# Kernel optimization log

Measured on AMD Instinct MI355X. Metric: run time of the kernel, lower is better.

## Reference

```python
import jax, jax.numpy as jnp
import numpy as np

DIM = 1024
HEADS = 16
HEAD_DIM = DIM // HEADS
B, N = 4, 4096


def setup_inputs() -> dict:
    key = jax.random.key(0)
    ks = jax.random.split(key, 10)
    s = 1.0 / np.sqrt(DIM)
    return {
        "x": jax.random.normal(ks[0], (B, N, DIM), dtype=jnp.float32),
        "Wq": jax.random.uniform(ks[1], (DIM, DIM), jnp.float32, -s, s),
        "bq": jax.random.uniform(ks[2], (DIM,), jnp.float32, -s, s),
        "Wk": jax.random.uniform(ks[3], (DIM, DIM), jnp.float32, -s, s),
        "bk": jax.random.uniform(ks[4], (DIM,), jnp.float32, -s, s),
        "Wv": jax.random.uniform(ks[5], (DIM, DIM), jnp.float32, -s, s),
        "bv": jax.random.uniform(ks[6], (DIM,), jnp.float32, -s, s),
        "Wo": jax.random.uniform(ks[7], (DIM, DIM), jnp.float32, -s, s),
        "bo": jax.random.uniform(ks[8], (DIM,), jnp.float32, -s, s),
        "stdp": jnp.ones((HEADS,), dtype=jnp.float32),
    }


def reference(x, Wq, bq, Wk, bk, Wv, bv, Wo, bo, stdp):
    b, n, d = x.shape
    h, dh = HEADS, HEAD_DIM
    # projections (torch Linear: x @ W.T + b)
    def proj(W, bias):
        return (x @ W.T + bias).reshape(b, n, h, dh).transpose(0, 2, 1, 3)  # bhnd
    Q = jax.nn.elu(proj(Wq, bq)) + 1.0
    K = jax.nn.elu(proj(Wk, bk)) + 1.0
    V = proj(Wv, bv)
    stdp_w = jax.nn.sigmoid(stdp).reshape(1, h, 1, 1)
    KV = jnp.einsum('bhnd,bhnv->bhdv', K, V)      # (b,h,dh,dh)
    K_sum = K.sum(axis=2)                          # (b,h,dh)
    numerator = jnp.einsum('bhnd,bhdv->bhnv', Q, KV)
    denominator = jnp.einsum('bhnd,bhd->bhn', Q, K_sum)[..., None] + 1e-6
    attn_out = numerator / denominator * stdp_w    # (b,h,n,dh)
    out = attn_out.transpose(0, 2, 1, 3).reshape(b, n, d)
    out = out @ Wo.T + bo
    return (out, jax.lax.stop_gradient(stdp))
```

## Files before the change

### kernel.cpp

```cpp
#include <hip/hip_runtime.h>
#include <hip/hip_bf16.h>

#define DIMSZ 1024
#define SEQLEN 4096
#define NHEAD 16
#define NX 16777216L
#define NW 1048576L
#define KVSPLITS 8

typedef __attribute__((ext_vector_type(8))) short bf16x8;
typedef __attribute__((ext_vector_type(4))) float f32x4;

__device__ __forceinline__ unsigned short f2bf(float f) {
    union { float f; unsigned int i; } c; c.f = f;
    unsigned int x = c.i;
    unsigned int r = (x + 0x7fffu + ((x >> 16) & 1u)) >> 16;
    return (unsigned short)r;
}

__device__ __forceinline__ unsigned int pk2(float lo, float hi) {
    union { float f; unsigned int i; } a, b; a.f = lo; b.f = hi;
    return __builtin_amdgcn_perm(b.i + 0x8000u, a.i + 0x8000u, 0x07060302u);
}

__device__ __forceinline__ void unp8r(bf16x8 v, float* f) {
    union { bf16x8 s; uint4 w; } u; u.s = v;
    union { unsigned int i; float f; } c;
    c.i = u.w.x << 16;           f[0] = c.f;
    c.i = u.w.x & 0xffff0000u;   f[1] = c.f;
    c.i = u.w.y << 16;           f[2] = c.f;
    c.i = u.w.y & 0xffff0000u;   f[3] = c.f;
    c.i = u.w.z << 16;           f[4] = c.f;
    c.i = u.w.z & 0xffff0000u;   f[5] = c.f;
    c.i = u.w.w << 16;           f[6] = c.f;
    c.i = u.w.w & 0xffff0000u;   f[7] = c.f;
}

__device__ __forceinline__ void async16(const void* g, void* l) {
    __builtin_amdgcn_global_load_lds(
        (const __attribute__((address_space(1))) void*)g,
        (__attribute__((address_space(3))) void*)l,
        16, 0, 0);
}

__global__ __launch_bounds__(256) void cast_pack(
    const float* __restrict__ x, const float* __restrict__ Wq,
    const float* __restrict__ Wk, const float* __restrict__ Wv,
    const float* __restrict__ Wo, const float* __restrict__ stdp,
    unsigned short* __restrict__ xb, unsigned short* __restrict__ Wqkv,
    unsigned short* __restrict__ Wob, float* __restrict__ outTail)
{
    long i4 = ((long)blockIdx.x * 256 + threadIdx.x) * 4;
    const float* src; unsigned short* dst; long off;
    if (i4 < NX)               { src = x;  dst = xb;          off = i4; }
    else if (i4 < NX + NW)     { src = Wq; dst = Wqkv;        off = i4 - NX; }
    else if (i4 < NX + 2*NW)   { src = Wk; dst = Wqkv + NW;   off = i4 - NX - NW; }
    else if (i4 < NX + 3*NW)   { src = Wv; dst = Wqkv + 2*NW; off = i4 - NX - 2*NW; }
    else                       { src = Wo; dst = Wob;         off = i4 - NX - 3*NW; }
    float4 v = *(const float4*)(src + off);
    union { unsigned short u[4]; uint2 p; } o;
    o.u[0] = f2bf(v.x); o.u[1] = f2bf(v.y); o.u[2] = f2bf(v.z); o.u[3] = f2bf(v.w);
    *(uint2*)(dst + off) = o.p;
    if (blockIdx.x == 0 && threadIdx.x < NHEAD) outTail[threadIdx.x] = stdp[threadIdx.x];
}

__global__ __launch_bounds__(1024, 1) void qkv_gemm8(
    const unsigned short* __restrict__ A, const unsigned short* __restrict__ W,
    const float* __restrict__ bq, const float* __restrict__ bk,
    const float* __restrict__ bv,
    unsigned short* __restrict__ Qb, unsigned short* __restrict__ Kb,
    unsigned short* __restrict__ Vb)
{
    __shared__ __align__(16) char SM[131072];
    const int t = threadIdx.x;
    const int wave = t >> 6, lane = t & 63;
    const int lr = lane & 15, lq = lane >> 4;
    const int wm = wave >> 2, wn = wave & 3;
    const int m0 = blockIdx.x * 256;
    const int c0 = blockIdx.y * 256;

    const int sc = (((t & 7) ^ ((t >> 3) & 7)) * 8);
    const unsigned short* pA = A + (long)(m0 + (t >> 3)) * DIMSZ + sc;
    const unsigned short* pB = W + (long)(c0 + (t >> 3)) * DIMSZ + sc;
    char* ldsW = SM + wave * 1024;

    const int xo = ((lq ^ (lr & 7)) << 4);
    const char* ABase = SM + wm * 8192 + lr * 128;
    const char* BBase = SM + 32768 + (wn * 64 + lr) * 128;

    f32x4 acc[4][4];
    #pragma unroll
    for (int i = 0; i < 4; ++i)
        #pragma unroll
        for (int j = 0; j < 4; ++j) acc[i][j] = (f32x4){0.f, 0.f, 0.f, 0.f};

#define STAGE(Q, O) do {                                                        \
        if ((Q) < 16) {                                                         \
            const int isB_ = ((O) < 2) ? 1 : 0;                                 \
            const int half_ = isB_ ? (O) : ((O) - 2);                           \
            const unsigned short* s_ = (isB_ ? pB : pA)                         \
                                       + (long)half_ * 131072 + (Q) * 64;       \
            char* d_ = ldsW + (((Q) & 1) << 16) + isB_ * 32768 + half_ * 16384; \
            async16(s_, d_);                                                    \
        }                                                                       \
    } while (0)

    STAGE(0, 0); STAGE(0, 1); STAGE(0, 2); STAGE(0, 3);
    STAGE(1, 0); STAGE(1, 1); STAGE(1, 2);
    asm volatile("s_waitcnt vmcnt(3)" ::: "memory");
    __builtin_amdgcn_s_barrier();

    for (int kt = 0; kt < 16; ++kt) {
        const int buf = (kt & 1) << 16;
        bf16x8 a[4], b[4];

        b[0] = *(const bf16x8*)(BBase + buf + 0 * 2048 + xo);
        b[1] = *(const bf16x8*)(BBase + buf + 1 * 2048 + xo);
        #pragma unroll
        for (int i = 0; i < 4; ++i)
            a[i] = *(const bf16x8*)(ABase + buf + i * 2048 + xo);
        __builtin_amdgcn_sched_barrier(0);
        b[2] = *(const bf16x8*)(BBase + buf + 2 * 2048 + xo);
        b[3] = *(const bf16x8*)(BBase + buf + 3 * 2048 + xo);
        __builtin_amdgcn_sched_barrier(0);
        STAGE(kt + 1, 3);

        asm volatile("s_waitcnt lgkmcnt(2)" ::: "memory");
        __builtin_amdgcn_sched_barrier(0);
        __builtin_amdgcn_s_setprio(1);
        #pragma unroll
        for (int i = 0; i < 4; ++i)
            #pragma unroll
            for (int j = 0; j < 2; ++j)
                acc[i][j] = __builtin_amdgcn_mfma_f32_16x16x32_bf16(
                    b[j], a[i], acc[i][j], 0, 0, 0);
        __builtin_amdgcn_s_setprio(0);

        asm volatile("s_waitcnt lgkmcnt(0)" ::: "memory");
        __builtin_amdgcn_sched_barrier(0);
        __builtin_amdgcn_s_setprio(1);
        #pragma unroll
        for (int i = 0; i < 4; ++i)
            #pragma unroll
            for (int j = 2; j < 4; ++j)
                acc[i][j] = __builtin_amdgcn_mfma_f32_16x16x32_bf16(
                    b[j], a[i], acc[i][j], 0, 0, 0);
        __builtin_amdgcn_s_setprio(0);

        b[0] = *(const bf16x8*)(BBase + buf + 0 * 2048 + (xo ^ 64));
        b[1] = *(const bf16x8*)(BBase + buf + 1 * 2048 + (xo ^ 64));
        #pragma unroll
        for (int i = 0; i < 4; ++i)
            a[i] = *(const bf16x8*)(ABase + buf + i * 2048 + (xo ^ 64));
        __builtin_amdgcn_sched_barrier(0);
        b[2] = *(const bf16x8*)(BBase + buf + 2 * 2048 + (xo ^ 64));
        b[3] = *(const bf16x8*)(BBase + buf + 3 * 2048 + (xo ^ 64));
        __builtin_amdgcn_sched_barrier(0);

        asm volatile("s_waitcnt lgkmcnt(2)" ::: "memory");
        __builtin_amdgcn_sched_barrier(0);
        __builtin_amdgcn_s_setprio(1);
        #pragma unroll
        for (int i = 0; i < 4; ++i)
            #pragma unroll
            for (int j = 0; j < 2; ++j)
                acc[i][j] = __builtin_amdgcn_mfma_f32_16x16x32_bf16(
                    b[j], a[i], acc[i][j], 0, 0, 0);
        __builtin_amdgcn_s_setprio(0);

        asm volatile("s_waitcnt lgkmcnt(0)" ::: "memory");
        __builtin_amdgcn_sched_barrier(0);
        __builtin_amdgcn_s_barrier();
        STAGE(kt + 2, 0); STAGE(kt + 2, 1); STAGE(kt + 2, 2);

        __builtin_amdgcn_s_setprio(1);
        #pragma unroll
        for (int i = 0; i < 4; ++i)
            #pragma unroll
            for (int j = 2; j < 4; ++j)
                acc[i][j] = __builtin_amdgcn_mfma_f32_16x16x32_bf16(
                    b[j], a[i], acc[i][j], 0, 0, 0);
        __builtin_amdgcn_s_setprio(0);

        if (kt < 14)       asm volatile("s_waitcnt vmcnt(3)" ::: "memory");
        else if (kt == 14) asm volatile("s_waitcnt vmcnt(0)" ::: "memory");
        __builtin_amdgcn_s_barrier();
    }
#undef STAGE

    const int proj = c0 >> 10;
    const float* bias = proj == 0 ? bq : (proj == 1 ? bk : bv);
    const bool qk = proj < 2;
    const int cb = (c0 & 1023) + wn * 64;
    const int q4 = lq * 4;
    #pragma unroll
    for (int j = 0; j < 4; ++j) {
        const float4 b4 = *(const float4*)(bias + cb + 16 * j + q4);
        #pragma unroll
        for (int i = 0; i < 4; ++i) {
            float v0 = acc[i][j][0] + b4.x, v1 = acc[i][j][1] + b4.y;
            float v2 = acc[i][j][2] + b4.z, v3 = acc[i][j][3] + b4.w;
            if (qk) {
                v0 = v0 > 0.f ? v0 + 1.f : __expf(v0);
                v1 = v1 > 0.f ? v1 + 1.f : __expf(v1);
                v2 = v2 > 0.f ? v2 + 1.f : __expf(v2);
                v3 = v3 > 0.f ? v3 + 1.f : __expf(v3);
            }
            const int row = wm * 64 + 16 * i + lr;
            int byte = row * 512 + wn * 128 + j * 32 + q4 * 2;
            byte ^= (row & 7) << 4;
            uint2 pkd; pkd.x = pk2(v0, v1); pkd.y = pk2(v2, v3);
            *(uint2*)(SM + byte) = pkd;
        }
    }
    __syncthreads();
    unsigned short* dstp = proj == 0 ? Qb : (proj == 1 ? Kb : Vb);
    const int colsh = (t & 31) * 8;
    const int h = ((c0 >> 6) + (colsh >> 6)) & 15;
    const int b_ = m0 >> 12;
    unsigned short* dbase = dstp + ((long)(b_ * 16 + h) * SEQLEN) * 64 + (colsh & 63);
    #pragma unroll
    for (int u = 0; u < 8; ++u) {
        const int flat = u * 16384 + t * 16;
        const int row = flat >> 9;
        uint4 val = *(const uint4*)(SM + (flat ^ ((row & 7) << 4)));
        const int n = (m0 + row) & 4095;
        *(uint4*)(dbase + (long)n * 64) = val;
    }
}

__global__ __launch_bounds__(256) void kv_reduce(
    const unsigned short* __restrict__ Kb, const unsigned short* __restrict__ Vb,
    float* __restrict__ KVp, float* __restrict__ Ksump)
{
    __shared__ __align__(16) char LDS[65536];
    int bh = blockIdx.x, split = blockIdx.y, t = threadIdx.x;
    int wave = t >> 6, lane = t & 63, lr = lane & 15, lq = lane >> 4;

    const int nl = t & 127;
    const int dh = (t >> 7) * 32;
    const int vrow = 16 * wave + lr;

    f32x4 acc[4];
    #pragma unroll
    for (int j = 0; j < 4; ++j) acc[j] = (f32x4){0.f, 0.f, 0.f, 0.f};
    float ksp[4] = {0.f, 0.f, 0.f, 0.f};

    for (int half = 0; half < 2; ++half) {
        const unsigned short* Kbase = Kb + ((long)bh * SEQLEN + split * 512 + half * 256) * 64;
        const unsigned short* Vbase = Vb + ((long)bh * SEQLEN + split * 512 + half * 256) * 64;

        union Q2S { uint4 q[4]; unsigned short s[32]; };
        Q2S kq[2], vq[2];
        #pragma unroll
        for (int it = 0; it < 2; ++it) {
            const unsigned short* kp = Kbase + (long)(it * 128 + nl) * 64 + dh;
            const unsigned short* vp = Vbase + (long)(it * 128 + nl) * 64 + dh;
            #pragma unroll
            for (int g = 0; g < 4; ++g) {
                kq[it].q[g] = *(const uint4*)(kp + g * 8);
                vq[it].q[g] = *(const uint4*)(vp + g * 8);
            }
        }
        if (half) __syncthreads();
        #pragma unroll
        for (int it = 0; it < 2; ++it) {
            char* buf = LDS + it * 32768;
            #pragma unroll
            for (int e = 0; e < 32; ++e) {
                const int d = dh + e;
                const int a = d * 256 + ((nl * 2) ^ ((d & 7) << 4));
                *(unsigned short*)(buf + a) = kq[it].s[e];
                *(unsigned short*)(buf + 16384 + a) = vq[it].s[e];
            }
        }
        __syncthreads();

        #pragma unroll
        for (int it = 0; it < 2; ++it) {
            const char* buf = LDS + it * 32768;
            #pragma unroll
            for (int ns = 0; ns < 4; ++ns) {
                const int xoff = (ns * 64 + lq * 16) ^ ((lr & 7) << 4);
                bf16x8 af = *(const bf16x8*)(buf + 16384 + vrow * 256 + xoff);
                bf16x8 bfr[4];
                #pragma unroll
                for (int j = 0; j < 4; ++j)
                    bfr[j] = *(const bf16x8*)(buf + (16 * j + lr) * 256 + xoff);
                if (wave == 0) {
                    #pragma unroll
                    for (int j = 0; j < 4; ++j) {
                        float kf[8]; unp8r(bfr[j], kf);
                        ksp[j] += ((kf[0] + kf[1]) + (kf[2] + kf[3]))
                                + ((kf[4] + kf[5]) + (kf[6] + kf[7]));
                    }
                }
                #pragma unroll
                for (int j = 0; j < 4; ++j)
                    acc[j] = __builtin_amdgcn_mfma_f32_16x16x32_bf16(bfr[j], af, acc[j], 0, 0, 0);
            }
        }
    }

    float* kp = KVp + ((long)split * 64 + bh) * 4096;
    const int q4 = lq * 4;
    #pragma unroll
    for (int j = 0; j < 4; ++j)
        *(f32x4*)(kp + vrow * 64 + 16 * j + q4) = acc[j];

    if (wave == 0) {
        #pragma unroll
        for (int j = 0; j < 4; ++j) {
            float s = ksp[j];
            s += __shfl_xor(s, 16);
            s += __shfl_xor(s, 32);
            if (lane < 16)
                Ksump[((long)split * 64 + bh) * 64 + 16 * j + lr] = s;
        }
    }
}

__global__ __launch_bounds__(256) void kv_final(
    const float* __restrict__ KVp, const float* __restrict__ Ksump,
    unsigned short* __restrict__ KVb, float* __restrict__ Ksum)
{
    int bh = blockIdx.x, t = threadIdx.x;
    float s[16];
    #pragma unroll
    for (int g = 0; g < 16; ++g) s[g] = 0.f;
    for (int sp = 0; sp < KVSPLITS; ++sp) {
        const float* src = KVp + ((long)sp * 64 + bh) * 4096 + t * 16;
        #pragma unroll
        for (int g = 0; g < 4; ++g) {
            float4 v = *(const float4*)(src + g * 4);
            s[g * 4 + 0] += v.x; s[g * 4 + 1] += v.y;
            s[g * 4 + 2] += v.z; s[g * 4 + 3] += v.w;
        }
    }
    uint4 o0, o1;
    o0.x = pk2(s[0], s[1]);  o0.y = pk2(s[2], s[3]);
    o0.z = pk2(s[4], s[5]);  o0.w = pk2(s[6], s[7]);
    o1.x = pk2(s[8], s[9]);  o1.y = pk2(s[10], s[11]);
    o1.z = pk2(s[12], s[13]); o1.w = pk2(s[14], s[15]);
    *(uint4*)(KVb + (long)bh * 4096 + t * 16) = o0;
    *(uint4*)(KVb + (long)bh * 4096 + t * 16 + 8) = o1;
    if (t < 16) {
        float4 a = {0.f, 0.f, 0.f, 0.f};
        for (int p = 0; p < KVSPLITS; p += 4) {
            #pragma unroll
            for (int q = 0; q < 4; ++q) {
                float4 v = *(const float4*)(Ksump + ((long)(p + q) * 64 + bh) * 64 + t * 4);
                a.x += v.x; a.y += v.y; a.z += v.z; a.w += v.w;
            }
        }
        *(float4*)(Ksum + bh * 64 + t * 4) = a;
    }
}

__global__ __launch_bounds__(256) void attn_kernel(
    const unsigned short* __restrict__ Qb, const unsigned short* __restrict__ KVb,
    const float* __restrict__ Ksum, const float* __restrict__ stdp,
    unsigned short* __restrict__ attn)
{
    __shared__ unsigned short Cs[256 * 72];
    int t = threadIdx.x;
    int bh = blockIdx.y;
    int b = bh >> 4, h = bh & 15;

    int wave = t >> 6, lane = t & 63, lr = lane & 15, lk = (lane >> 4) * 8;
    const unsigned short* kvb = KVb + (long)bh * 4096;
    const float* ksb = Ksum + bh * 64;

    bf16x8 bfrh[2][4];
    float ksf[2][8];
    #pragma unroll
    for (int s = 0; s < 2; ++s) {
        #pragma unroll
        for (int j = 0; j < 4; ++j)
            bfrh[s][j] = *(const bf16x8*)(kvb + (16 * j + lr) * 64 + s * 32 + lk);
        float4 ka = *(const float4*)(ksb + s * 32 + lk);
        float4 kb2 = *(const float4*)(ksb + s * 32 + lk + 4);
        ksf[s][0] = ka.x; ksf[s][1] = ka.y; ksf[s][2] = ka.z; ksf[s][3] = ka.w;
        ksf[s][4] = kb2.x; ksf[s][5] = kb2.y; ksf[s][6] = kb2.z; ksf[s][7] = kb2.w;
    }
    float sg = 1.f / (1.f + __expf(-stdp[h]));
    int q4 = (lane >> 4) * 4;

    for (int c = 0; c < 2; ++c) {
        int rc = blockIdx.x * 2 + c;
        int rowbase = rc * 256 + wave * 64;

        f32x4 acc[4][4];
        #pragma unroll
        for (int i = 0; i < 4; ++i)
            #pragma unroll
            for (int j = 0; j < 4; ++j) acc[i][j] = (f32x4){0.f, 0.f, 0.f, 0.f};
        float ds[4] = {0.f, 0.f, 0.f, 0.f};

        #pragma unroll
        for (int s = 0; s < 2; ++s) {
            bf16x8 af[4];
            #pragma unroll
            for (int i = 0; i < 4; ++i)
                af[i] = *(const bf16x8*)(Qb + ((long)bh * SEQLEN + rowbase + 16 * i + lr) * 64 + s * 32 + lk);
            #pragma unroll
            for (int i = 0; i < 4; ++i) {
                float qf[8]; unp8r(af[i], qf);
                #pragma unroll
                for (int e = 0; e < 8; ++e) ds[i] += qf[e] * ksf[s][e];
            }
            #pragma unroll
            for (int i = 0; i < 4; ++i)
                #pragma unroll
                for (int j = 0; j < 4; ++j)
                    acc[i][j] = __builtin_amdgcn_mfma_f32_16x16x32_bf16(bfrh[s][j], af[i], acc[i][j], 0, 0, 0);
        }

        float dinv_i[4];
        #pragma unroll
        for (int i = 0; i < 4; ++i) {
            float d = ds[i];
            d += __shfl_xor(d, 16);
            d += __shfl_xor(d, 32);
            dinv_i[i] = sg / (d + 1e-6f);
        }

        #pragma unroll
        for (int j = 0; j < 4; ++j) {
            int v0c = 16 * j + q4;
            #pragma unroll
            for (int i = 0; i < 4; ++i) {
                int row = wave * 64 + 16 * i + lr;
                float d = dinv_i[i];
                uint2 pkd;
                pkd.x = pk2(acc[i][j][0] * d, acc[i][j][1] * d);
                pkd.y = pk2(acc[i][j][2] * d, acc[i][j][3] * d);
                *(uint2*)(Cs + row * 72 + v0c) = pkd;
            }
        }
        __syncthreads();
        #pragma unroll
        for (int u = 0; u < 8; ++u) {
            int row = u * 32 + (t >> 3);
            int nn = rc * 256 + row;
            long a = ((long)(b * SEQLEN + nn)) * DIMSZ + h * 64 + (t & 7) * 8;
            *(uint4*)(attn + a) = *(const uint4*)(Cs + row * 72 + (t & 7) * 8);
        }
        __syncthreads();
    }
}

__global__ __launch_bounds__(1024, 1) void out_gemm8(
    const unsigned short* __restrict__ A, const unsigned short* __restrict__ W,
    const float* __restrict__ bo, float* __restrict__ out)
{
    __shared__ __align__(16) char SM[131072];
    const int t = threadIdx.x;
    const int wave = t >> 6, lane = t & 63;
    const int lr = lane & 15, lq = lane >> 4;
    const int wm = wave >> 2, wn = wave & 3;
    const int m0 = blockIdx.x * 256;
    const int c0 = blockIdx.y * 256;

    const int sc = (((t & 7) ^ ((t >> 3) & 7)) * 8);
    const unsigned short* pA = A + (long)(m0 + (t >> 3)) * DIMSZ + sc;
    const unsigned short* pB = W + (long)(c0 + (t >> 3)) * DIMSZ + sc;
    char* ldsW = SM + wave * 1024;

    const int xo = ((lq ^ (lr & 7)) << 4);
    const char* ABase = SM + wm * 8192 + lr * 128;
    const char* BBase = SM + 32768 + (wn * 64 + lr) * 128;

    f32x4 acc[4][4];
    #pragma unroll
    for (int i = 0; i < 4; ++i)
        #pragma unroll
        for (int j = 0; j < 4; ++j) acc[i][j] = (f32x4){0.f, 0.f, 0.f, 0.f};

#define STAGE(Q, O) do {                                                        \
        if ((Q) < 16) {                                                         \
            const int isB_ = ((O) < 2) ? 1 : 0;                                 \
            const int half_ = isB_ ? (O) : ((O) - 2);                           \
            const unsigned short* s_ = (isB_ ? pB : pA)                         \
                                       + (long)half_ * 131072 + (Q) * 64;       \
            char* d_ = ldsW + (((Q) & 1) << 16) + isB_ * 32768 + half_ * 16384; \
            async16(s_, d_);                                                    \
        }                                                                       \
    } while (0)

    STAGE(0, 0); STAGE(0, 1); STAGE(0, 2); STAGE(0, 3);
    STAGE(1, 0); STAGE(1, 1); STAGE(1, 2);
    asm volatile("s_waitcnt vmcnt(3)" ::: "memory");
    __builtin_amdgcn_s_barrier();

    for (int kt = 0; kt < 16; ++kt) {
        const int buf = (kt & 1) << 16;
        bf16x8 a[4], b[4];

        b[0] = *(const bf16x8*)(BBase + buf + 0 * 2048 + xo);
        b[1] = *(const bf16x8*)(BBase + buf + 1 * 2048 + xo);
        #pragma unroll
        for (int i = 0; i < 4; ++i)
            a[i] = *(const bf16x8*)(ABase + buf + i * 2048 + xo);
        __builtin_amdgcn_sched_barrier(0);
        b[2] = *(const bf16x8*)(BBase + buf + 2 * 2048 + xo);
        b[3] = *(const bf16x8*)(BBase + buf + 3 * 2048 + xo);
        __builtin_amdgcn_sched_barrier(0);
        STAGE(kt + 1, 3);

        asm volatile("s_waitcnt lgkmcnt(2)" ::: "memory");
        __builtin_amdgcn_sched_barrier(0);
        __builtin_amdgcn_s_setprio(1);
        #pragma unroll
        for (int i = 0; i < 4; ++i)
            #pragma unroll
            for (int j = 0; j < 2; ++j)
                acc[i][j] = __builtin_amdgcn_mfma_f32_16x16x32_bf16(
                    b[j], a[i], acc[i][j], 0, 0, 0);
        __builtin_amdgcn_s_setprio(0);

        asm volatile("s_waitcnt lgkmcnt(0)" ::: "memory");
        __builtin_amdgcn_sched_barrier(0);
        __builtin_amdgcn_s_setprio(1);
        #pragma unroll
        for (int i = 0; i < 4; ++i)
            #pragma unroll
            for (int j = 2; j < 4; ++j)
                acc[i][j] = __builtin_amdgcn_mfma_f32_16x16x32_bf16(
                    b[j], a[i], acc[i][j], 0, 0, 0);
        __builtin_amdgcn_s_setprio(0);

        b[0] = *(const bf16x8*)(BBase + buf + 0 * 2048 + (xo ^ 64));
        b[1] = *(const bf16x8*)(BBase + buf + 1 * 2048 + (xo ^ 64));
        #pragma unroll
        for (int i = 0; i < 4; ++i)
            a[i] = *(const bf16x8*)(ABase + buf + i * 2048 + (xo ^ 64));
        __builtin_amdgcn_sched_barrier(0);
        b[2] = *(const bf16x8*)(BBase + buf + 2 * 2048 + (xo ^ 64));
        b[3] = *(const bf16x8*)(BBase + buf + 3 * 2048 + (xo ^ 64));
        __builtin_amdgcn_sched_barrier(0);

        asm volatile("s_waitcnt lgkmcnt(2)" ::: "memory");
        __builtin_amdgcn_sched_barrier(0);
        __builtin_amdgcn_s_setprio(1);
        #pragma unroll
        for (int i = 0; i < 4; ++i)
            #pragma unroll
            for (int j = 0; j < 2; ++j)
                acc[i][j] = __builtin_amdgcn_mfma_f32_16x16x32_bf16(
                    b[j], a[i], acc[i][j], 0, 0, 0);
        __builtin_amdgcn_s_setprio(0);

        asm volatile("s_waitcnt lgkmcnt(0)" ::: "memory");
        __builtin_amdgcn_sched_barrier(0);
        __builtin_amdgcn_s_barrier();
        STAGE(kt + 2, 0); STAGE(kt + 2, 1); STAGE(kt + 2, 2);

        __builtin_amdgcn_s_setprio(1);
        #pragma unroll
        for (int i = 0; i < 4; ++i)
            #pragma unroll
            for (int j = 2; j < 4; ++j)
                acc[i][j] = __builtin_amdgcn_mfma_f32_16x16x32_bf16(
                    b[j], a[i], acc[i][j], 0, 0, 0);
        __builtin_amdgcn_s_setprio(0);

        if (kt < 14)       asm volatile("s_waitcnt vmcnt(3)" ::: "memory");
        else if (kt == 14) asm volatile("s_waitcnt vmcnt(0)" ::: "memory");
        __builtin_amdgcn_s_barrier();
    }
#undef STAGE

    const int q4 = lq * 4;
    #pragma unroll
    for (int j = 0; j < 4; ++j) {
        const int c = c0 + wn * 64 + 16 * j + q4;
        const float4 b4 = *(const float4*)(bo + c);
        #pragma unroll
        for (int i = 0; i < 4; ++i) {
            const int gm = m0 + wm * 64 + 16 * i + lr;
            float4 v;
            v.x = acc[i][j][0] + b4.x; v.y = acc[i][j][1] + b4.y;
            v.z = acc[i][j][2] + b4.z; v.w = acc[i][j][3] + b4.w;
            *(float4*)(out + (long)gm * DIMSZ + c) = v;
        }
    }
}

extern "C" void kernel_launch(void* const* d_in, const int* in_sizes, int n_in,
                              void* d_out, int out_size, void* d_ws, size_t ws_size,
                              hipStream_t stream) {
    const float* x    = (const float*)d_in[0];
    const float* Wq   = (const float*)d_in[1];
    const float* bq   = (const float*)d_in[2];
    const float* Wk   = (const float*)d_in[3];
    const float* bk   = (const float*)d_in[4];
    const float* Wv   = (const float*)d_in[5];
    const float* bv   = (const float*)d_in[6];
    const float* Wo   = (const float*)d_in[7];
    const float* bo   = (const float*)d_in[8];
    const float* stdp = (const float*)d_in[9];
    float* out = (float*)d_out;

    char* ws = (char*)d_ws;
    unsigned short* xb   = (unsigned short*)(ws);
    float*          KVp  = (float*)(ws);
    unsigned short* attn = (unsigned short*)(ws);
    unsigned short* Wqkv = (unsigned short*)(ws + 33554432L);
    float*          Ksump= (float*)(ws + 33554432L);
    unsigned short* KVb  = (unsigned short*)(ws + 33816576L);
    float*          Ksum = (float*)(ws + 34340864L);
    unsigned short* Wob  = (unsigned short*)(ws + 39845888L);
    unsigned short* Qb   = (unsigned short*)(ws + 41943040L);
    unsigned short* Kb   = (unsigned short*)(ws + 75497472L);
    unsigned short* Vb   = (unsigned short*)(ws + 109051904L);

    cast_pack<<<20480, 256, 0, stream>>>(x, Wq, Wk, Wv, Wo, stdp, xb, Wqkv, Wob,
                                         out + 16777216L);
    qkv_gemm8<<<dim3(64, 12), 1024, 0, stream>>>(xb, Wqkv, bq, bk, bv, Qb, Kb, Vb);
    kv_reduce<<<dim3(64, KVSPLITS), 256, 0, stream>>>(Kb, Vb, KVp, Ksump);
    kv_final<<<64, 256, 0, stream>>>(KVp, Ksump, KVb, Ksum);
    attn_kernel<<<dim3(8, 64), 256, 0, stream>>>(Qb, KVb, Ksum, stdp, attn);
    out_gemm8<<<dim3(64, 4), 1024, 0, stream>>>(attn, Wob, bo, out);
}
```

Baseline: 312.2 us.

## Load QKV GEMM A operand directly from global, halve LDS footprint

The QKV projection GEMM no longer stages the activation tile A through LDS. Each wave loads its A fragments directly from global memory into registers, and only the weight tile B is double-buffered in LDS, which halves shared memory to 64 KB. The epilogue is split into two passes to fit the smaller buffer, and launch bounds now request more occupancy. The risk is that direct global A loads are uncoalesced and are waited on with vmcnt(0) every iteration, which exposes global latency and removes prefetch overlap for A.

New measurement: 446.6 us. +43.0%, slower.

```diff
diff --git a/kernel.cpp b/kernel.cpp
--- a/kernel.cpp
+++ b/kernel.cpp
@@ -64,14 +64,14 @@
     if (blockIdx.x == 0 && threadIdx.x < NHEAD) outTail[threadIdx.x] = stdp[threadIdx.x];
 }
 
-__global__ __launch_bounds__(1024, 1) void qkv_gemm8(
+__global__ __launch_bounds__(1024, 4) void qkv_gemm8(
     const unsigned short* __restrict__ A, const unsigned short* __restrict__ W,
     const float* __restrict__ bq, const float* __restrict__ bk,
     const float* __restrict__ bv,
     unsigned short* __restrict__ Qb, unsigned short* __restrict__ Kb,
     unsigned short* __restrict__ Vb)
 {
-    __shared__ __align__(16) char SM[131072];
+    __shared__ __align__(16) char SM[65536];
     const int t = threadIdx.x;
     const int wave = t >> 6, lane = t & 63;
     const int lr = lane & 15, lq = lane >> 4;
@@ -80,13 +80,12 @@
     const int c0 = blockIdx.y * 256;
 
     const int sc = (((t & 7) ^ ((t >> 3) & 7)) * 8);
-    const unsigned short* pA = A + (long)(m0 + (t >> 3)) * DIMSZ + sc;
     const unsigned short* pB = W + (long)(c0 + (t >> 3)) * DIMSZ + sc;
-    char* ldsW = SM + wave * 1024;
+
+    const unsigned short* pAW = A + (long)(m0 + wm * 64 + lr) * DIMSZ + lq * 8;
 
     const int xo = ((lq ^ (lr & 7)) << 4);
-    const char* ABase = SM + wm * 8192 + lr * 128;
-    const char* BBase = SM + 32768 + (wn * 64 + lr) * 128;
+    const char* BB = SM + (wn * 64 + lr) * 128;
 
     f32x4 acc[4][4];
     #pragma unroll
@@ -94,138 +93,137 @@
         #pragma unroll
         for (int j = 0; j < 4; ++j) acc[i][j] = (f32x4){0.f, 0.f, 0.f, 0.f};
 
-#define STAGE(Q, O) do {                                                        \
+#define STAGEB(Q, H) do {                                                       \
         if ((Q) < 16) {                                                         \
-            const int isB_ = ((O) < 2) ? 1 : 0;                                 \
-            const int half_ = isB_ ? (O) : ((O) - 2);                           \
-            const unsigned short* s_ = (isB_ ? pB : pA)                         \
-                                       + (long)half_ * 131072 + (Q) * 64;       \
-            char* d_ = ldsW + (((Q) & 1) << 16) + isB_ * 32768 + half_ * 16384; \
+            const unsigned short* s_ = pB + (long)(H) * 131072 + (Q) * 64;      \
+            char* d_ = SM + (((Q) & 1) << 15) + (H) * 16384 + wave * 1024;      \
             async16(s_, d_);                                                    \
         }                                                                       \
     } while (0)
 
-    STAGE(0, 0); STAGE(0, 1); STAGE(0, 2); STAGE(0, 3);
-    STAGE(1, 0); STAGE(1, 1); STAGE(1, 2);
-    asm volatile("s_waitcnt vmcnt(3)" ::: "memory");
+    STAGEB(0, 0); STAGEB(0, 1);
+    STAGEB(1, 0); STAGEB(1, 1);
+    asm volatile("s_waitcnt vmcnt(0)" ::: "memory");
     __builtin_amdgcn_s_barrier();
 
     for (int kt = 0; kt < 16; ++kt) {
-        const int buf = (kt & 1) << 16;
-        bf16x8 a[4], b[4];
-
-        b[0] = *(const bf16x8*)(BBase + buf + 0 * 2048 + xo);
-        b[1] = *(const bf16x8*)(BBase + buf + 1 * 2048 + xo);
-        #pragma unroll
-        for (int i = 0; i < 4; ++i)
-            a[i] = *(const bf16x8*)(ABase + buf + i * 2048 + xo);
-        __builtin_amdgcn_sched_barrier(0);
-        b[2] = *(const bf16x8*)(BBase + buf + 2 * 2048 + xo);
-        b[3] = *(const bf16x8*)(BBase + buf + 3 * 2048 + xo);
-        __builtin_amdgcn_sched_barrier(0);
-        STAGE(kt + 1, 3);
-
+        const int bo = (kt & 1) << 15;
+        bf16x8 a[4][2];
+        bf16x8 b0, b1, b2, b3;
+
+        #pragma unroll
+        for (int i = 0; i < 4; ++i) {
+            a[i][0] = *(const bf16x8*)(pAW + i * 16384 + kt * 64);
+            a[i][1] = *(const bf16x8*)(pAW + i * 16384 + kt * 64 + 32);
+        }
+        __builtin_amdgcn_sched_barrier(0);
+
+        b0 = *(const bf16x8*)(BB + bo + 0 * 2048 + xo);
+        b1 = *(const bf16x8*)(BB + bo + 1 * 2048 + xo);
+        __builtin_amdgcn_sched_barrier(0);
+        b2 = *(const bf16x8*)(BB + bo + 2 * 2048 + xo);
+        b3 = *(const bf16x8*)(BB + bo + 3 * 2048 + xo);
+        __builtin_amdgcn_sched_barrier(0);
+
+        asm volatile("s_waitcnt vmcnt(0)" ::: "memory");
         asm volatile("s_waitcnt lgkmcnt(2)" ::: "memory");
         __builtin_amdgcn_sched_barrier(0);
         __builtin_amdgcn_s_setprio(1);
         #pragma unroll
-        for (int i = 0; i < 4; ++i)
-            #pragma unroll
-            for (int j = 0; j < 2; ++j)
-                acc[i][j] = __builtin_amdgcn_mfma_f32_16x16x32_bf16(
-                    b[j], a[i], acc[i][j], 0, 0, 0);
+        for (int i = 0; i < 4; ++i) {
+            acc[i][0] = __builtin_amdgcn_mfma_f32_16x16x32_bf16(b0, a[i][0], acc[i][0], 0, 0, 0);
+            acc[i][1] = __builtin_amdgcn_mfma_f32_16x16x32_bf16(b1, a[i][0], acc[i][1], 0, 0, 0);
+        }
         __builtin_amdgcn_s_setprio(0);
 
         asm volatile("s_waitcnt lgkmcnt(0)" ::: "memory");
         __builtin_amdgcn_sched_barrier(0);
         __builtin_amdgcn_s_setprio(1);
         #pragma unroll
-        for (int i = 0; i < 4; ++i)
-            #pragma unroll
-            for (int j = 2; j < 4; ++j)
-                acc[i][j] = __builtin_amdgcn_mfma_f32_16x16x32_bf16(
-                    b[j], a[i], acc[i][j], 0, 0, 0);
-        __builtin_amdgcn_s_setprio(0);
-
-        b[0] = *(const bf16x8*)(BBase + buf + 0 * 2048 + (xo ^ 64));
-        b[1] = *(const bf16x8*)(BBase + buf + 1 * 2048 + (xo ^ 64));
-        #pragma unroll
-        for (int i = 0; i < 4; ++i)
-            a[i] = *(const bf16x8*)(ABase + buf + i * 2048 + (xo ^ 64));
-        __builtin_amdgcn_sched_barrier(0);
-        b[2] = *(const bf16x8*)(BBase + buf + 2 * 2048 + (xo ^ 64));
-        b[3] = *(const bf16x8*)(BBase + buf + 3 * 2048 + (xo ^ 64));
+        for (int i = 0; i < 4; ++i) {
+            acc[i][2] = __builtin_amdgcn_mfma_f32_16x16x32_bf16(b2, a[i][0], acc[i][2], 0, 0, 0);
+            acc[i][3] = __builtin_amdgcn_mfma_f32_16x16x32_bf16(b3, a[i][0], acc[i][3], 0, 0, 0);
+        }
+        __builtin_amdgcn_s_setprio(0);
+
+        b0 = *(const bf16x8*)(BB + bo + 0 * 2048 + (xo ^ 64));
+        b1 = *(const bf16x8*)(BB + bo + 1 * 2048 + (xo ^ 64));
+        __builtin_amdgcn_sched_barrier(0);
+        b2 = *(const bf16x8*)(BB + bo + 2 * 2048 + (xo ^ 64));
+        b3 = *(const bf16x8*)(BB + bo + 3 * 2048 + (xo ^ 64));
         __builtin_amdgcn_sched_barrier(0);
 
         asm volatile("s_waitcnt lgkmcnt(2)" ::: "memory");
         __builtin_amdgcn_sched_barrier(0);
         __builtin_amdgcn_s_setprio(1);
         #pragma unroll
-        for (int i = 0; i < 4; ++i)
-            #pragma unroll
-            for (int j = 0; j < 2; ++j)
-                acc[i][j] = __builtin_amdgcn_mfma_f32_16x16x32_bf16(
-                    b[j], a[i], acc[i][j], 0, 0, 0);
+        for (int i = 0; i < 4; ++i) {
+            acc[i][0] = __builtin_amdgcn_mfma_f32_16x16x32_bf16(b0, a[i][1], acc[i][0], 0, 0, 0);
+            acc[i][1] = __builtin_amdgcn_mfma_f32_16x16x32_bf16(b1, a[i][1], acc[i][1], 0, 0, 0);
+        }
         __builtin_amdgcn_s_setprio(0);
 
         asm volatile("s_waitcnt lgkmcnt(0)" ::: "memory");
         __builtin_amdgcn_sched_barrier(0);
         __builtin_amdgcn_s_barrier();
-        STAGE(kt + 2, 0); STAGE(kt + 2, 1); STAGE(kt + 2, 2);
-
-        __builtin_amdgcn_s_setprio(1);
-        #pragma unroll
-        for (int i = 0; i < 4; ++i)
-            #pragma unroll
-            for (int j = 2; j < 4; ++j)
-                acc[i][j] = __builtin_amdgcn_mfma_f32_16x16x32_bf16(
-                    b[j], a[i], acc[i][j], 0, 0, 0);
-        __builtin_amdgcn_s_setprio(0);
-
-        if (kt < 14)       asm volatile("s_waitcnt vmcnt(3)" ::: "memory");
-        else if (kt == 14) asm volatile("s_waitcnt vmcnt(0)" ::: "memory");
+        STAGEB(kt + 2, 0); STAGEB(kt + 2, 1);
+
+        __builtin_amdgcn_s_setprio(1);
+        #pragma unroll
+        for (int i = 0; i < 4; ++i) {
+            acc[i][2] = __builtin_amdgcn_mfma_f32_16x16x32_bf16(b2, a[i][1], acc[i][2], 0, 0, 0);
+            acc[i][3] = __builtin_amdgcn_mfma_f32_16x16x32_bf16(b3, a[i][1], acc[i][3], 0, 0, 0);
+        }
+        __builtin_amdgcn_s_setprio(0);
         __builtin_amdgcn_s_barrier();
     }
-#undef STAGE
+#undef STAGEB
 
     const int proj = c0 >> 10;
     const float* bias = proj == 0 ? bq : (proj == 1 ? bk : bv);
     const bool qk = proj < 2;
     const int cb = (c0 & 1023) + wn * 64;
     const int q4 = lq * 4;
-    #pragma unroll
-    for (int j = 0; j < 4; ++j) {
-        const float4 b4 = *(const float4*)(bias + cb + 16 * j + q4);
-        #pragma unroll
-        for (int i = 0; i < 4; ++i) {
-            float v0 = acc[i][j][0] + b4.x, v1 = acc[i][j][1] + b4.y;
-            float v2 = acc[i][j][2] + b4.z, v3 = acc[i][j][3] + b4.w;
-            if (qk) {
-                v0 = v0 > 0.f ? v0 + 1.f : __expf(v0);
-                v1 = v1 > 0.f ? v1 + 1.f : __expf(v1);
-                v2 = v2 > 0.f ? v2 + 1.f : __expf(v2);
-                v3 = v3 > 0.f ? v3 + 1.f : __expf(v3);
-            }
-            const int row = wm * 64 + 16 * i + lr;
-            int byte = row * 512 + wn * 128 + j * 32 + q4 * 2;
-            byte ^= (row & 7) << 4;
-            uint2 pkd; pkd.x = pk2(v0, v1); pkd.y = pk2(v2, v3);
-            *(uint2*)(SM + byte) = pkd;
-        }
-    }
-    __syncthreads();
     unsigned short* dstp = proj == 0 ? Qb : (proj == 1 ? Kb : Vb);
     const int colsh = (t & 31) * 8;
     const int h = ((c0 >> 6) + (colsh >> 6)) & 15;
     const int b_ = m0 >> 12;
     unsigned short* dbase = dstp + ((long)(b_ * 16 + h) * SEQLEN) * 64 + (colsh & 63);
-    #pragma unroll
-    for (int u = 0; u < 8; ++u) {
-        const int flat = u * 16384 + t * 16;
-        const int row = flat >> 9;
-        uint4 val = *(const uint4*)(SM + (flat ^ ((row & 7) << 4)));
-        const int n = (m0 + row) & 4095;
-        *(uint4*)(dbase + (long)n * 64) = val;
+
+    #pragma unroll
+    for (int p = 0; p < 2; ++p) {
+        __syncthreads();
+        if ((wm >> 1) == p) {
+            #pragma unroll
+            for (int j = 0; j < 4; ++j) {
+                const float4 b4 = *(const float4*)(bias + cb + 16 * j + q4);
+                #pragma unroll
+                for (int i = 0; i < 4; ++i) {
+                    float v0 = acc[i][j][0] + b4.x, v1 = acc[i][j][1] + b4.y;
+                    float v2 = acc[i][j][2] + b4.z, v3 = acc[i][j][3] + b4.w;
+                    if (qk) {
+                        v0 = v0 > 0.f ? v0 + 1.f : __expf(v0);
+                        v1 = v1 > 0.f ? v1 + 1.f : __expf(v1);
+                        v2 = v2 > 0.f ? v2 + 1.f : __expf(v2);
+                        v3 = v3 > 0.f ? v3 + 1.f : __expf(v3);
+                    }
+                    const int lrow = (wm & 1) * 64 + 16 * i + lr;
+                    int byte = lrow * 512 + wn * 128 + j * 32 + q4 * 2;
+                    byte ^= (lrow & 7) << 4;
+                    uint2 pkd; pkd.x = pk2(v0, v1); pkd.y = pk2(v2, v3);
+                    *(uint2*)(SM + byte) = pkd;
+                }
+            }
+        }
+        __syncthreads();
+        #pragma unroll
+        for (int u = 0; u < 4; ++u) {
+            const int flat = u * 16384 + t * 16;
+            const int lrow = flat >> 9;
+            uint4 val = *(const uint4*)(SM + (flat ^ ((lrow & 7) << 4)));
+            const int n = (m0 + p * 128 + lrow) & 4095;
+            *(uint4*)(dbase + (long)n * 64) = val;
+        }
     }
 }
 
```
